# Kernel tuning notes

Measured on AMD Instinct MI355X. Metric: run time of the kernel, lower is better.

The kernel has to match this reference:

```python
import jax, jax.numpy as jnp
import numpy as np

N_NODES = 50000
N_EDGES = 400000


def setup_inputs() -> dict:
    key = jax.random.key(0)
    ks = jax.random.split(key, 8)
    d_in, d_hid, d_out = 512, 512, 256
    feats = jax.random.normal(ks[0], (N_NODES, d_in), dtype=jnp.float32)
    src = jax.random.randint(ks[1], (N_EDGES,), 0, N_NODES, dtype=jnp.int32)
    dst = jax.random.randint(ks[2], (N_EDGES,), 0, N_NODES, dtype=jnp.int32)
    # Glorot-ish scaled weights so activations stay O(1)
    W0 = jax.random.normal(ks[3], (d_in, d_hid), dtype=jnp.float32) / np.sqrt(d_in)
    b0 = jnp.zeros((d_hid,), jnp.float32)
    W1 = jax.random.normal(ks[4], (d_hid, d_hid), dtype=jnp.float32) / np.sqrt(d_hid)
    b1 = jnp.zeros((d_hid,), jnp.float32)
    W2 = jax.random.normal(ks[5], (d_hid, d_out), dtype=jnp.float32) / np.sqrt(d_hid)
    b2 = jnp.zeros((d_out,), jnp.float32)
    return {"feats": feats, "src": src, "dst": dst,
            "W0": W0, "b0": b0, "W1": W1, "b1": b1, "W2": W2, "b2": b2}


def _sage_conv_gcn(h, src, dst, W, b, deg):
    # DGL SAGEConv aggregator_type='gcn':
    # h_neigh[v] = (sum_{u->v} h[u] + h[v]) / (in_deg(v) + 1); out = h_neigh @ W + b
    agg = jax.ops.segment_sum(h[src], dst, num_segments=h.shape[0])  # [N, d]
    h_neigh = (agg + h) / (deg[:, None] + 1.0)
    return h_neigh @ W + b


def reference(feats, src, dst, W0, b0, W1, b1, W2, b2):
    N = feats.shape[0]
    deg = jax.ops.segment_sum(jnp.ones((src.shape[0],), feats.dtype), dst,
                              num_segments=N)  # in-degree per node
    h = jax.nn.relu(_sage_conv_gcn(feats, src, dst, W0, b0, deg))  # dropout p=0, norm none
    h = jax.nn.relu(_sage_conv_gcn(h, src, dst, W1, b1, deg))
    h = _sage_conv_gcn(h, src, dst, W2, b2, deg)  # final layer: no activation
    return h
```

## Files before the change

### kernel.cpp

```cpp
#include <hip/hip_runtime.h>
#include <stdint.h>

#define N_NODES 50000
#define N_EDGES 400000
#define MPAD    50048
#define SCAN_B  49

typedef __bf16 bf16x8 __attribute__((ext_vector_type(8)));
typedef float  f32x4  __attribute__((ext_vector_type(4)));
typedef unsigned short ushort_t;
typedef unsigned int   uint_t;

__device__ __forceinline__ ushort_t f2b(float f){
    uint_t x = __float_as_uint(f);
    x += 0x7FFFu + ((x >> 16) & 1u);
    return (ushort_t)(x >> 16);
}
__device__ __forceinline__ float b2f(ushort_t h){
    return __uint_as_float(((uint_t)h) << 16);
}

__device__ __forceinline__ int xcd_swz(int orig, int nwg){
    int q = nwg >> 3, r = nwg & 7;
    int xcd = orig & 7, idx = orig >> 3;
    int base = (xcd < r) ? xcd * (q + 1) : r * (q + 1) + (xcd - r) * q;
    return base + idx;
}

__global__ void zero_two(int* a, int* b, int n){
    int i = blockIdx.x * blockDim.x + threadIdx.x;
    if (i < n){ a[i] = 0; b[i] = 0; }
}

__global__ void hist_kernel(const int* __restrict__ dst, int* __restrict__ deg, int E){
    int i = blockIdx.x * blockDim.x + threadIdx.x;
    if (i < E) atomicAdd(&deg[dst[i]], 1);
}

__global__ __launch_bounds__(1024) void blk_scan_kernel(
        const int* __restrict__ deg, int* __restrict__ offs,
        int* __restrict__ bsum, int n){
    __shared__ int buf[1024];
    const int t = threadIdx.x, b = blockIdx.x;
    const int i = b * 1024 + t;
    int v = (i < n) ? deg[i] : 0;
    buf[t] = v; __syncthreads();
    for (int off = 1; off < 1024; off <<= 1){
        int x = (t >= off) ? buf[t - off] : 0;
        __syncthreads();
        buf[t] += x;
        __syncthreads();
    }
    if (i < n) offs[i] = buf[t] - v;
    if (t == 1023) bsum[b] = buf[1023];
}

__global__ void bsum_scan_kernel(int* __restrict__ bsum, int nb){
    int t = threadIdx.x;
    int orig = (t < nb) ? bsum[t] : 0;
    int v = orig;
    #pragma unroll
    for (int off = 1; off < 64; off <<= 1){
        int x = __shfl_up(v, off, 64);
        if (t >= off) v += x;
    }
    if (t < nb) bsum[t] = v - orig;
}

__global__ __launch_bounds__(1024) void add_off_kernel(
        int* __restrict__ offs, const int* __restrict__ bsum, int n){
    int i = blockIdx.x * 1024 + threadIdx.x;
    if (i < n) offs[i] += bsum[blockIdx.x];
    if (i == 0) offs[n] = N_EDGES;
}

__global__ void fill_kernel(const int* __restrict__ src, const int* __restrict__ dst,
                            const int* __restrict__ offs, int* __restrict__ cursor,
                            int* __restrict__ nbr, int E){
    int i = blockIdx.x * blockDim.x + threadIdx.x;
    if (i < E){
        int d = dst[i];
        int p = atomicAdd(&cursor[d], 1);
        nbr[offs[d] + p] = src[i];
    }
}

__global__ __launch_bounds__(256) void wtrans_kernel(const float* __restrict__ W,
                                                     ushort_t* __restrict__ Wt,
                                                     int K, int N){
    __shared__ float t[32][33];
    const int bx = blockIdx.x * 32;
    const int by = blockIdx.y * 32;
    const int x = threadIdx.x & 31, y = threadIdx.x >> 5;
    #pragma unroll
    for (int j = 0; j < 32; j += 8)
        t[y + j][x] = W[(size_t)(by + y + j) * N + bx + x];
    __syncthreads();
    #pragma unroll
    for (int j = 0; j < 32; j += 8)
        Wt[(size_t)(bx + y + j) * K + by + x] = f2b(t[x][y + j]);
}

__device__ __forceinline__ void load16(const void* g, void* l){
    __builtin_amdgcn_global_load_lds((const __attribute__((address_space(1))) void*)g,
                                     (__attribute__((address_space(3))) void*)l, 16, 0, 0);
}

__global__ __launch_bounds__(256, 4) void gemm128_bt(const ushort_t* __restrict__ A,
                                                     const ushort_t* __restrict__ Bt,
                                                     ushort_t* __restrict__ C,
                                                     int NBN, int N, int K){
    __shared__ ushort_t As[128 * 64];
    __shared__ ushort_t Bs[128 * 64];
    const int tid  = threadIdx.x, lane = tid & 63, wave = tid >> 6;
    const int wg = xcd_swz(blockIdx.x, gridDim.x);
    const int bm = wg / NBN, bn = wg - bm * NBN;
    const int fr = lane & 15;
    const int wm = (wave >> 1) * 64, wn = (wave & 1) * 64;
    f32x4 acc[4][4] = {};

    for (int kt = 0; kt < K; kt += 64){
        __syncthreads();
        #pragma unroll
        for (int i = 0; i < 4; i++){
            int s = tid + i * 256;
            int row = s >> 3, p = s & 7, c = p ^ (row & 7);
            load16(A + (size_t)(bm * 128 + row) * K + kt + c * 8,
                   (char*)As + s * 16);
        }
        #pragma unroll
        for (int i = 0; i < 4; i++){
            int s = tid + i * 256;
            int row = s >> 3, p = s & 7, c = p ^ (row & 7);
            load16(Bt + (size_t)(bn * 128 + row) * K + kt + c * 8,
                   (char*)Bs + s * 16);
        }
        __syncthreads();
        #pragma unroll
        for (int ks = 0; ks < 2; ks++){
            const int c = (lane >> 4) + ks * 4;
            const int cx = c ^ (fr & 7);
            bf16x8 af[4], bf[4];
            #pragma unroll
            for (int t = 0; t < 4; t++)
                af[t] = *(const bf16x8*)(const void*)(As + (wm + t * 16 + fr) * 64 + cx * 8);
            #pragma unroll
            for (int t = 0; t < 4; t++)
                bf[t] = *(const bf16x8*)(const void*)(Bs + (wn + t * 16 + fr) * 64 + cx * 8);
            #pragma unroll
            for (int tm = 0; tm < 4; tm++)
                #pragma unroll
                for (int tn = 0; tn < 4; tn++)
                    acc[tm][tn] = __builtin_amdgcn_mfma_f32_16x16x32_bf16(
                                      af[tm], bf[tn], acc[tm][tn], 0, 0, 0);
        }
    }
    const int r0 = (lane >> 4) * 4, c0 = lane & 15;
    #pragma unroll
    for (int tm = 0; tm < 4; tm++){
        #pragma unroll
        for (int tn = 0; tn < 4; tn++){
            int rbase = bm * 128 + wm + tm * 16 + r0;
            int cidx  = bn * 128 + wn + tn * 16 + c0;
            #pragma unroll
            for (int reg = 0; reg < 4; reg++)
                C[(size_t)(rbase + reg) * N + cidx] = f2b(acc[tm][tn][reg]);
        }
    }
}

__global__ __launch_bounds__(256, 4) void gemm128_a32(const float* __restrict__ A,
                                                      const ushort_t* __restrict__ Bt,
                                                      ushort_t* __restrict__ C,
                                                      int K){
    __shared__ ushort_t As[128 * 64];
    __shared__ ushort_t Bs[128 * 64];
    const int tid  = threadIdx.x, lane = tid & 63, wave = tid >> 6;
    const int wg = xcd_swz(blockIdx.x, gridDim.x);
    const int bm = wg >> 2, bn = wg & 3;
    const int fr = lane & 15;
    const int wm = (wave >> 1) * 64, wn = (wave & 1) * 64;
    f32x4 acc[4][4] = {};

    for (int kt = 0; kt < K; kt += 64){
        __syncthreads();
        float4 x[4], y[4];
        #pragma unroll
        for (int i = 0; i < 4; i++){
            int s = tid + i * 256;
            int row = s >> 3, p = s & 7, c = p ^ (row & 7);
            int grow = bm * 128 + row;
            if (grow < N_NODES){
                const float* pp = A + (size_t)grow * K + kt + c * 8;
                x[i] = *(const float4*)(const void*)pp;
                y[i] = *(const float4*)(const void*)(pp + 4);
            } else {
                x[i] = make_float4(0.f, 0.f, 0.f, 0.f);
                y[i] = make_float4(0.f, 0.f, 0.f, 0.f);
            }
        }
        #pragma unroll
        for (int i = 0; i < 4; i++){
            int s = tid + i * 256;
            int row = s >> 3, p = s & 7, c = p ^ (row & 7);
            load16(Bt + (size_t)(bn * 128 + row) * K + kt + c * 8,
                   (char*)Bs + s * 16);
        }
        #pragma unroll
        for (int i = 0; i < 4; i++){
            int s = tid + i * 256;
            uint4 o;
            o.x = (uint_t)f2b(x[i].x) | ((uint_t)f2b(x[i].y) << 16);
            o.y = (uint_t)f2b(x[i].z) | ((uint_t)f2b(x[i].w) << 16);
            o.z = (uint_t)f2b(y[i].x) | ((uint_t)f2b(y[i].y) << 16);
            o.w = (uint_t)f2b(y[i].z) | ((uint_t)f2b(y[i].w) << 16);
            *(uint4*)(void*)((char*)As + s * 16) = o;
        }
        __syncthreads();
        #pragma unroll
        for (int ks = 0; ks < 2; ks++){
            const int c = (lane >> 4) + ks * 4;
            const int cx = c ^ (fr & 7);
            bf16x8 af[4], bf[4];
            #pragma unroll
            for (int t = 0; t < 4; t++)
                af[t] = *(const bf16x8*)(const void*)(As + (wm + t * 16 + fr) * 64 + cx * 8);
            #pragma unroll
            for (int t = 0; t < 4; t++)
                bf[t] = *(const bf16x8*)(const void*)(Bs + (wn + t * 16 + fr) * 64 + cx * 8);
            #pragma unroll
            for (int tm = 0; tm < 4; tm++)
                #pragma unroll
                for (int tn = 0; tn < 4; tn++)
                    acc[tm][tn] = __builtin_amdgcn_mfma_f32_16x16x32_bf16(
                                      af[tm], bf[tn], acc[tm][tn], 0, 0, 0);
        }
    }
    const int r0 = (lane >> 4) * 4, c0 = lane & 15;
    #pragma unroll
    for (int tm = 0; tm < 4; tm++){
        #pragma unroll
        for (int tn = 0; tn < 4; tn++){
            int rbase = bm * 128 + wm + tm * 16 + r0;
            int cidx  = bn * 128 + wn + tn * 16 + c0;
            #pragma unroll
            for (int reg = 0; reg < 4; reg++)
                C[(size_t)(rbase + reg) * 512 + cidx] = f2b(acc[tm][tn][reg]);
        }
    }
}

__device__ __forceinline__ void acc8(float* a, uint4 y){
    a[0] += b2f((ushort_t)(y.x & 0xffff)); a[1] += b2f((ushort_t)(y.x >> 16));
    a[2] += b2f((ushort_t)(y.y & 0xffff)); a[3] += b2f((ushort_t)(y.y >> 16));
    a[4] += b2f((ushort_t)(y.z & 0xffff)); a[5] += b2f((ushort_t)(y.z >> 16));
    a[6] += b2f((ushort_t)(y.w & 0xffff)); a[7] += b2f((ushort_t)(y.w >> 16));
}
__device__ __forceinline__ void acc4(float* a, uint2 y){
    a[0] += b2f((ushort_t)(y.x & 0xffff)); a[1] += b2f((ushort_t)(y.x >> 16));
    a[2] += b2f((ushort_t)(y.y & 0xffff)); a[3] += b2f((ushort_t)(y.y >> 16));
}

__global__ __launch_bounds__(256) void agg_relu_kernel(
        const ushort_t* __restrict__ Y, const int* __restrict__ offs,
        const int* __restrict__ nbr, const float* __restrict__ bias,
        ushort_t* __restrict__ H){
    const int lane = threadIdx.x & 63, wave = threadIdx.x >> 6;
    const int v = blockIdx.x * 4 + wave;
    const int off = lane * 8;
    float a[8];
    {   uint4 y = *(const uint4*)(const void*)(Y + (size_t)v * 512 + off);
        a[0] = b2f((ushort_t)(y.x & 0xffff)); a[1] = b2f((ushort_t)(y.x >> 16));
        a[2] = b2f((ushort_t)(y.y & 0xffff)); a[3] = b2f((ushort_t)(y.y >> 16));
        a[4] = b2f((ushort_t)(y.z & 0xffff)); a[5] = b2f((ushort_t)(y.z >> 16));
        a[6] = b2f((ushort_t)(y.w & 0xffff)); a[7] = b2f((ushort_t)(y.w >> 16)); }
    const int beg = offs[v], end = offs[v + 1];
    int i = beg;
    for (; i + 8 <= end; i += 8){
        uint4 yy[8];
        #pragma unroll
        for (int j = 0; j < 8; j++){
            int u = nbr[i + j];
            yy[j] = *(const uint4*)(const void*)(Y + (size_t)u * 512 + off);
        }
        #pragma unroll
        for (int j = 0; j < 8; j++) acc8(a, yy[j]);
    }
    for (; i + 4 <= end; i += 4){
        uint4 yy[4];
        #pragma unroll
        for (int j = 0; j < 4; j++){
            int u = nbr[i + j];
            yy[j] = *(const uint4*)(const void*)(Y + (size_t)u * 512 + off);
        }
        #pragma unroll
        for (int j = 0; j < 4; j++) acc8(a, yy[j]);
    }
    for (; i < end; i++){
        int u = nbr[i];
        uint4 y = *(const uint4*)(const void*)(Y + (size_t)u * 512 + off);
        acc8(a, y);
    }
    const float inv = 1.0f / (float)(end - beg + 1);
    float4 bb0 = ((const float4*)bias)[lane * 2];
    float4 bb1 = ((const float4*)bias)[lane * 2 + 1];
    float r[8];
    r[0] = a[0]*inv + bb0.x; r[1] = a[1]*inv + bb0.y;
    r[2] = a[2]*inv + bb0.z; r[3] = a[3]*inv + bb0.w;
    r[4] = a[4]*inv + bb1.x; r[5] = a[5]*inv + bb1.y;
    r[6] = a[6]*inv + bb1.z; r[7] = a[7]*inv + bb1.w;
    #pragma unroll
    for (int j = 0; j < 8; j++) r[j] = r[j] > 0.f ? r[j] : 0.f;
    uint4 o;
    o.x = (uint_t)f2b(r[0]) | ((uint_t)f2b(r[1]) << 16);
    o.y = (uint_t)f2b(r[2]) | ((uint_t)f2b(r[3]) << 16);
    o.z = (uint_t)f2b(r[4]) | ((uint_t)f2b(r[5]) << 16);
    o.w = (uint_t)f2b(r[6]) | ((uint_t)f2b(r[7]) << 16);
    *(uint4*)(void*)(H + (size_t)v * 512 + off) = o;
}

__global__ __launch_bounds__(256) void agg_out_kernel(
        const ushort_t* __restrict__ Y, const int* __restrict__ offs,
        const int* __restrict__ nbr, const float* __restrict__ bias,
        float* __restrict__ out){
    const int lane = threadIdx.x & 63, wave = threadIdx.x >> 6;
    const int v = blockIdx.x * 4 + wave;
    const int off = lane * 4;
    float a[4];
    {   uint2 y = *(const uint2*)(const void*)(Y + (size_t)v * 256 + off);
        a[0] = b2f((ushort_t)(y.x & 0xffff)); a[1] = b2f((ushort_t)(y.x >> 16));
        a[2] = b2f((ushort_t)(y.y & 0xffff)); a[3] = b2f((ushort_t)(y.y >> 16)); }
    const int beg = offs[v], end = offs[v + 1];
    int i = beg;
    for (; i + 8 <= end; i += 8){
        uint2 yy[8];
        #pragma unroll
        for (int j = 0; j < 8; j++){
            int u = nbr[i + j];
            yy[j] = *(const uint2*)(const void*)(Y + (size_t)u * 256 + off);
        }
        #pragma unroll
        for (int j = 0; j < 8; j++) acc4(a, yy[j]);
    }
    for (; i + 4 <= end; i += 4){
        uint2 yy[4];
        #pragma unroll
        for (int j = 0; j < 4; j++){
            int u = nbr[i + j];
            yy[j] = *(const uint2*)(const void*)(Y + (size_t)u * 256 + off);
        }
        #pragma unroll
        for (int j = 0; j < 4; j++) acc4(a, yy[j]);
    }
    for (; i < end; i++){
        int u = nbr[i];
        uint2 y = *(const uint2*)(const void*)(Y + (size_t)u * 256 + off);
        acc4(a, y);
    }
    const float inv = 1.0f / (float)(end - beg + 1);
    float4 bb = ((const float4*)bias)[lane];
    float4 r;
    r.x = a[0]*inv + bb.x; r.y = a[1]*inv + bb.y;
    r.z = a[2]*inv + bb.z; r.w = a[3]*inv + bb.w;
    ((float4*)out)[v * 64 + lane] = r;
}

extern "C" void kernel_launch(void* const* d_in, const int* in_sizes, int n_in,
                              void* d_out, int out_size, void* d_ws, size_t ws_size,
                              hipStream_t stream) {
    const float* feats = (const float*)d_in[0];
    const int*   src   = (const int*)  d_in[1];
    const int*   dst   = (const int*)  d_in[2];
    const float* W0    = (const float*)d_in[3];
    const float* b0    = (const float*)d_in[4];
    const float* W1    = (const float*)d_in[5];
    const float* b1    = (const float*)d_in[6];
    const float* W2    = (const float*)d_in[7];
    const float* b2    = (const float*)d_in[8];
    float* out = (float*)d_out;

    char* w = (char*)d_ws;
    ushort_t* Abuf = (ushort_t*)w;  w += (size_t)MPAD * 512 * 2;
    ushort_t* Ybuf = (ushort_t*)w;  w += (size_t)MPAD * 512 * 2;
    ushort_t* W0t  = (ushort_t*)w;  w += 512 * 512 * 2;
    ushort_t* W1t  = (ushort_t*)w;  w += 512 * 512 * 2;
    ushort_t* W2t  = (ushort_t*)w;  w += 256 * 512 * 2;
    int* deg    = (int*)w;          w += 50048 * 4;
    int* offs   = (int*)w;          w += 50056 * 4;
    int* cursor = (int*)w;          w += 50048 * 4;
    int* nbr    = (int*)w;          w += (size_t)N_EDGES * 4;
    int* bsum   = (int*)w;          w += 64 * 4;

    zero_two<<<(N_NODES + 255) / 256, 256, 0, stream>>>(deg, cursor, N_NODES);
    hist_kernel<<<(N_EDGES + 255) / 256, 256, 0, stream>>>(dst, deg, N_EDGES);
    blk_scan_kernel<<<SCAN_B, 1024, 0, stream>>>(deg, offs, bsum, N_NODES);
    bsum_scan_kernel<<<1, 64, 0, stream>>>(bsum, SCAN_B);
    add_off_kernel<<<SCAN_B, 1024, 0, stream>>>(offs, bsum, N_NODES);
    fill_kernel<<<(N_EDGES + 255) / 256, 256, 0, stream>>>(src, dst, offs, cursor, nbr, N_EDGES);

    {
        dim3 gt0(512 / 32, 512 / 32);
        wtrans_kernel<<<gt0, 256, 0, stream>>>(W0, W0t, 512, 512);
        wtrans_kernel<<<gt0, 256, 0, stream>>>(W1, W1t, 512, 512);
        dim3 gt2(256 / 32, 512 / 32);
        wtrans_kernel<<<gt2, 256, 0, stream>>>(W2, W2t, 512, 256);
    }

    const int g01 = (MPAD / 128) * 4;
    const int g2  = (MPAD / 128) * 2;

    gemm128_a32<<<g01, 256, 0, stream>>>(feats, W0t, Ybuf, 512);
    agg_relu_kernel<<<N_NODES / 4, 256, 0, stream>>>(Ybuf, offs, nbr, b0, Abuf);
    gemm128_bt<<<g01, 256, 0, stream>>>(Abuf, W1t, Ybuf, 4, 512, 512);
    agg_relu_kernel<<<N_NODES / 4, 256, 0, stream>>>(Ybuf, offs, nbr, b1, Abuf);
    gemm128_bt<<<g2, 256, 0, stream>>>(Abuf, W2t, Ybuf, 2, 256, 512);
    agg_out_kernel<<<N_NODES / 4, 256, 0, stream>>>(Ybuf, offs, nbr, b2, out);
}
```

Baseline: 480.6 us.

## Widen layer-0/1 GEMM tiles to 128x256 and fuse weight transposes into one launch

The first two GEMMs (N=512) switch from 128x128 tiles with 256 threads to 128x256 tiles with 512 threads (8 waves). This halves how often each A row tile is re-read from global memory (two column blocks instead of four). For layer 0 it also halves the redundant fp32-to-bf16 conversion of the input features. The three weight-transpose launches are merged into a single kernel that dispatches on block index, saving two launches. The trade-off is more LDS per block and a different occupancy target, plus half as many workgroups in the grid.

```diff
diff --git a/kernel.cpp b/kernel.cpp
--- a/kernel.cpp
+++ b/kernel.cpp
@@ -85,12 +85,19 @@
     }
 }
 
-__global__ __launch_bounds__(256) void wtrans_kernel(const float* __restrict__ W,
-                                                     ushort_t* __restrict__ Wt,
-                                                     int K, int N){
+__global__ __launch_bounds__(256) void wtrans3_kernel(
+        const float* __restrict__ W0, const float* __restrict__ W1,
+        const float* __restrict__ W2, ushort_t* __restrict__ W0t,
+        ushort_t* __restrict__ W1t, ushort_t* __restrict__ W2t){
     __shared__ float t[32][33];
-    const int bx = blockIdx.x * 32;
-    const int by = blockIdx.y * 32;
+    int b = blockIdx.x;
+    const float* W; ushort_t* Wt; int K, N, bx, by;
+    if (b < 256){            W = W0; Wt = W0t; K = 512; N = 512;
+                             bx = (b & 15) * 32; by = (b >> 4) * 32; }
+    else if (b < 512){ b -= 256; W = W1; Wt = W1t; K = 512; N = 512;
+                             bx = (b & 15) * 32; by = (b >> 4) * 32; }
+    else {             b -= 512; W = W2; Wt = W2t; K = 512; N = 256;
+                             bx = (b & 7) * 32;  by = (b >> 3) * 32; }
     const int x = threadIdx.x & 31, y = threadIdx.x >> 5;
     #pragma unroll
     for (int j = 0; j < 32; j += 8)
@@ -104,6 +111,150 @@
 __device__ __forceinline__ void load16(const void* g, void* l){
     __builtin_amdgcn_global_load_lds((const __attribute__((address_space(1))) void*)g,
                                      (__attribute__((address_space(3))) void*)l, 16, 0, 0);
+}
+
+__global__ __launch_bounds__(512, 6) void gemm256_bt(const ushort_t* __restrict__ A,
+                                                     const ushort_t* __restrict__ Bt,
+                                                     ushort_t* __restrict__ C,
+                                                     int NBN, int N, int K){
+    __shared__ ushort_t As[128 * 64];
+    __shared__ ushort_t Bs[256 * 64];
+    const int tid  = threadIdx.x, lane = tid & 63, wave = tid >> 6;
+    const int wg = xcd_swz(blockIdx.x, gridDim.x);
+    const int bm = wg / NBN, bn = wg - bm * NBN;
+    const int fr = lane & 15;
+    const int wm = (wave >> 2) * 64, wn = (wave & 3) * 64;
+    f32x4 acc[4][4] = {};
+
+    for (int kt = 0; kt < K; kt += 64){
+        __syncthreads();
+        #pragma unroll
+        for (int i = 0; i < 2; i++){
+            int s = tid + i * 512;
+            int row = s >> 3, p = s & 7, c = p ^ (row & 7);
+            load16(A + (size_t)(bm * 128 + row) * K + kt + c * 8,
+                   (char*)As + s * 16);
+        }
+        #pragma unroll
+        for (int i = 0; i < 4; i++){
+            int s = tid + i * 512;
+            int row = s >> 3, p = s & 7, c = p ^ (row & 7);
+            load16(Bt + (size_t)(bn * 256 + row) * K + kt + c * 8,
+                   (char*)Bs + s * 16);
+        }
+        __syncthreads();
+        #pragma unroll
+        for (int ks = 0; ks < 2; ks++){
+            const int c = (lane >> 4) + ks * 4;
+            const int cx = c ^ (fr & 7);
+            bf16x8 af[4], bf[4];
+            #pragma unroll
+            for (int t = 0; t < 4; t++)
+                af[t] = *(const bf16x8*)(const void*)(As + (wm + t * 16 + fr) * 64 + cx * 8);
+            #pragma unroll
+            for (int t = 0; t < 4; t++)
+                bf[t] = *(const bf16x8*)(const void*)(Bs + (wn + t * 16 + fr) * 64 + cx * 8);
+            #pragma unroll
+            for (int tm = 0; tm < 4; tm++)
+                #pragma unroll
+                for (int tn = 0; tn < 4; tn++)
+                    acc[tm][tn] = __builtin_amdgcn_mfma_f32_16x16x32_bf16(
+                                      af[tm], bf[tn], acc[tm][tn], 0, 0, 0);
+        }
+    }
+    const int r0 = (lane >> 4) * 4, c0 = lane & 15;
+    #pragma unroll
+    for (int tm = 0; tm < 4; tm++){
+        #pragma unroll
+        for (int tn = 0; tn < 4; tn++){
+            int rbase = bm * 128 + wm + tm * 16 + r0;
+            int cidx  = bn * 256 + wn + tn * 16 + c0;
+            #pragma unroll
+            for (int reg = 0; reg < 4; reg++)
+                C[(size_t)(rbase + reg) * N + cidx] = f2b(acc[tm][tn][reg]);
+        }
+    }
+}
+
+__global__ __launch_bounds__(512, 6) void gemm256_a32(const float* __restrict__ A,
+                                                      const ushort_t* __restrict__ Bt,
+                                                      ushort_t* __restrict__ C,
+                                                      int K){
+    __shared__ ushort_t As[128 * 64];
+    __shared__ ushort_t Bs[256 * 64];
+    const int tid  = threadIdx.x, lane = tid & 63, wave = tid >> 6;
+    const int wg = xcd_swz(blockIdx.x, gridDim.x);
+    const int bm = wg >> 1, bn = wg & 1;
+    const int fr = lane & 15;
+    const int wm = (wave >> 2) * 64, wn = (wave & 3) * 64;
+    f32x4 acc[4][4] = {};
+
+    for (int kt = 0; kt < K; kt += 64){
+        __syncthreads();
+        float4 x[2], y[2];
+        #pragma unroll
+        for (int i = 0; i < 2; i++){
+            int s = tid + i * 512;
+            int row = s >> 3, p = s & 7, c = p ^ (row & 7);
+            int grow = bm * 128 + row;
+            if (grow < N_NODES){
+                const float* pp = A + (size_t)grow * K + kt + c * 8;
+                x[i] = *(const float4*)(const void*)pp;
+                y[i] = *(const float4*)(const void*)(pp + 4);
+            } else {
+                x[i] = make_float4(0.f, 0.f, 0.f, 0.f);
+                y[i] = make_float4(0.f, 0.f, 0.f, 0.f);
+            }
+        }
+        #pragma unroll
+        for (int i = 0; i < 4; i++){
+            int s = tid + i * 512;
+            int row = s >> 3, p = s & 7, c = p ^ (row & 7);
+            load16(Bt + (size_t)(bn * 256 + row) * K + kt + c * 8,
+                   (char*)Bs + s * 16);
+        }
+        #pragma unroll
+        for (int i = 0; i < 2; i++){
+            int s = tid + i * 512;
+            uint4 o;
+            o.x = (uint_t)f2b(x[i].x) | ((uint_t)f2b(x[i].y) << 16);
+            o.y = (uint_t)f2b(x[i].z) | ((uint_t)f2b(x[i].w) << 16);
+            o.z = (uint_t)f2b(y[i].x) | ((uint_t)f2b(y[i].y) << 16);
+            o.w = (uint_t)f2b(y[i].z) | ((uint_t)f2b(y[i].w) << 16);
+            *(uint4*)(void*)((char*)As + s * 16) = o;
+        }
+        __syncthreads();
+        #pragma unroll
+        for (int ks = 0; ks < 2; ks++){
+            const int c = (lane >> 4) + ks * 4;
+            const int cx = c ^ (fr & 7);
+            bf16x8 af[4], bf[4];
+            #pragma unroll
+            for (int t = 0; t < 4; t++)
+                af[t] = *(const bf16x8*)(const void*)(As + (wm + t * 16 + fr) * 64 + cx * 8);
+            #pragma unroll
+            for (int t = 0; t < 4; t++)
+                bf[t] = *(const bf16x8*)(const void*)(Bs + (wn + t * 16 + fr) * 64 + cx * 8);
+            #pragma unroll
+            for (int tm = 0; tm < 4; tm++)
+                #pragma unroll
+                for (int tn = 0; tn < 4; tn++)
+                    acc[tm][tn] = __builtin_amdgcn_mfma_f32_16x16x32_bf16(
+                                      af[tm], bf[tn], acc[tm][tn], 0, 0, 0);
+        }
+    }
+    const int r0 = (lane >> 4) * 4, c0 = lane & 15;
+    #pragma unroll
+    for (int tm = 0; tm < 4; tm++){
+        #pragma unroll
+        for (int tn = 0; tn < 4; tn++){
+            int rbase = bm * 128 + wm + tm * 16 + r0;
+            int cidx  = bn * 256 + wn + tn * 16 + c0;
+            #pragma unroll
+            for (int reg = 0; reg < 4; reg++)
+                C[(size_t)(rbase + reg) * 512 + cidx] = f2b(acc[tm][tn][reg]);
+        }
+    }
 }
 
 __global__ __launch_bounds__(256, 4) void gemm128_bt(const ushort_t* __restrict__ A,
@@ -165,87 +316,6 @@
             #pragma unroll
             for (int reg = 0; reg < 4; reg++)
                 C[(size_t)(rbase + reg) * N + cidx] = f2b(acc[tm][tn][reg]);
-        }
-    }
-}
-
-__global__ __launch_bounds__(256, 4) void gemm128_a32(const float* __restrict__ A,
-                                                      const ushort_t* __restrict__ Bt,
-                                                      ushort_t* __restrict__ C,
-                                                      int K){
-    __shared__ ushort_t As[128 * 64];
-    __shared__ ushort_t Bs[128 * 64];
-    const int tid  = threadIdx.x, lane = tid & 63, wave = tid >> 6;
-    const int wg = xcd_swz(blockIdx.x, gridDim.x);
-    const int bm = wg >> 2, bn = wg & 3;
-    const int fr = lane & 15;
-    const int wm = (wave >> 1) * 64, wn = (wave & 1) * 64;
-    f32x4 acc[4][4] = {};
-
-    for (int kt = 0; kt < K; kt += 64){
-        __syncthreads();
-        float4 x[4], y[4];
-        #pragma unroll
-        for (int i = 0; i < 4; i++){
-            int s = tid + i * 256;
-            int row = s >> 3, p = s & 7, c = p ^ (row & 7);
-            int grow = bm * 128 + row;
-            if (grow < N_NODES){
-                const float* pp = A + (size_t)grow * K + kt + c * 8;
-                x[i] = *(const float4*)(const void*)pp;
-                y[i] = *(const float4*)(const void*)(pp + 4);
-            } else {
-                x[i] = make_float4(0.f, 0.f, 0.f, 0.f);
-                y[i] = make_float4(0.f, 0.f, 0.f, 0.f);
-            }
-        }
-        #pragma unroll
-        for (int i = 0; i < 4; i++){
-            int s = tid + i * 256;
-            int row = s >> 3, p = s & 7, c = p ^ (row & 7);
-            load16(Bt + (size_t)(bn * 128 + row) * K + kt + c * 8,
-                   (char*)Bs + s * 16);
-        }
-        #pragma unroll
-        for (int i = 0; i < 4; i++){
-            int s = tid + i * 256;
-            uint4 o;
-            o.x = (uint_t)f2b(x[i].x) | ((uint_t)f2b(x[i].y) << 16);
-            o.y = (uint_t)f2b(x[i].z) | ((uint_t)f2b(x[i].w) << 16);
-            o.z = (uint_t)f2b(y[i].x) | ((uint_t)f2b(y[i].y) << 16);
-            o.w = (uint_t)f2b(y[i].z) | ((uint_t)f2b(y[i].w) << 16);
-            *(uint4*)(void*)((char*)As + s * 16) = o;
-        }
-        __syncthreads();
-        #pragma unroll
-        for (int ks = 0; ks < 2; ks++){
-            const int c = (lane >> 4) + ks * 4;
-            const int cx = c ^ (fr & 7);
-            bf16x8 af[4], bf[4];
-            #pragma unroll
-            for (int t = 0; t < 4; t++)
-                af[t] = *(const bf16x8*)(const void*)(As + (wm + t * 16 + fr) * 64 + cx * 8);
-            #pragma unroll
-            for (int t = 0; t < 4; t++)
-                bf[t] = *(const bf16x8*)(const void*)(Bs + (wn + t * 16 + fr) * 64 + cx * 8);
-            #pragma unroll
-            for (int tm = 0; tm < 4; tm++)
-                #pragma unroll
-                for (int tn = 0; tn < 4; tn++)
-                    acc[tm][tn] = __builtin_amdgcn_mfma_f32_16x16x32_bf16(
-                                      af[tm], bf[tn], acc[tm][tn], 0, 0, 0);
-        }
-    }
-    const int r0 = (lane >> 4) * 4, c0 = lane & 15;
-    #pragma unroll
-    for (int tm = 0; tm < 4; tm++){
-        #pragma unroll
-        for (int tn = 0; tn < 4; tn++){
-            int rbase = bm * 128 + wm + tm * 16 + r0;
-            int cidx  = bn * 128 + wn + tn * 16 + c0;
-            #pragma unroll
-            for (int reg = 0; reg < 4; reg++)
-                C[(size_t)(rbase + reg) * 512 + cidx] = f2b(acc[tm][tn][reg]);
         }
     }
 }
@@ -398,20 +468,14 @@
     add_off_kernel<<<SCAN_B, 1024, 0, stream>>>(offs, bsum, N_NODES);
     fill_kernel<<<(N_EDGES + 255) / 256, 256, 0, stream>>>(src, dst, offs, cursor, nbr, N_EDGES);
 
-    {
-        dim3 gt0(512 / 32, 512 / 32);
-        wtrans_kernel<<<gt0, 256, 0, stream>>>(W0, W0t, 512, 512);
-        wtrans_kernel<<<gt0, 256, 0, stream>>>(W1, W1t, 512, 512);
-        dim3 gt2(256 / 32, 512 / 32);
-        wtrans_kernel<<<gt2, 256, 0, stream>>>(W2, W2t, 512, 256);
-    }
-
-    const int g01 = (MPAD / 128) * 4;
+    wtrans3_kernel<<<640, 256, 0, stream>>>(W0, W1, W2, W0t, W1t, W2t);
+
+    const int g01 = (MPAD / 128) * 2;
     const int g2  = (MPAD / 128) * 2;
 
-    gemm128_a32<<<g01, 256, 0, stream>>>(feats, W0t, Ybuf, 512);
+    gemm256_a32<<<g01, 512, 0, stream>>>(feats, W0t, Ybuf, 512);
     agg_relu_kernel<<<N_NODES / 4, 256, 0, stream>>>(Ybuf, offs, nbr, b0, Abuf);
-    gemm128_bt<<<g01, 256, 0, stream>>>(Abuf, W1t, Ybuf, 4, 512, 512);
+    gemm256_bt<<<g01, 512, 0, stream>>>(Abuf, W1t, Ybuf, 2, 512, 512);
     agg_relu_kernel<<<N_NODES / 4, 256, 0, stream>>>(Ybuf, offs, nbr, b1, Abuf);
     gemm128_bt<<<g2, 256, 0, stream>>>(Abuf, W2t, Ybuf, 2, 256, 512);
     agg_out_kernel<<<N_NODES / 4, 256, 0, stream>>>(Ybuf, offs, nbr, b2, out);
```

Result: slower. 898.8 us (+87.0%).
